# Kernel tuning notes

Measured on AMD Instinct MI355X. Metric: run time of the kernel, lower is better.

Reference implementation:

```python
import jax, jax.numpy as jnp
import numpy as np

H = 16
D_MODEL = 1024
D_K = D_MODEL // H


def setup_inputs() -> dict:
    key = jax.random.key(0)
    ks = jax.random.split(key, 12)
    B, S = 4, 2048
    scale = 1.0 / np.sqrt(D_MODEL)
    inp = {
        "query": jax.random.normal(ks[0], (B, S, D_MODEL), dtype=jnp.float32),
        "key": jax.random.normal(ks[1], (B, S, D_MODEL), dtype=jnp.float32),
        "value": jax.random.normal(ks[2], (B, S, D_MODEL), dtype=jnp.float32),
        "Wq": jax.random.normal(ks[3], (D_MODEL, D_MODEL), dtype=jnp.float32) * scale,
        "bq": jnp.zeros((D_MODEL,), dtype=jnp.float32),
        "Wk": jax.random.normal(ks[4], (D_MODEL, D_MODEL), dtype=jnp.float32) * scale,
        "bk": jnp.zeros((D_MODEL,), dtype=jnp.float32),
        "Wv": jax.random.normal(ks[5], (D_MODEL, D_MODEL), dtype=jnp.float32) * scale,
        "bv": jnp.zeros((D_MODEL,), dtype=jnp.float32),
        "Wo": jax.random.normal(ks[6], (D_MODEL, D_MODEL), dtype=jnp.float32) * scale,
        "bo": jnp.zeros((D_MODEL,), dtype=jnp.float32),
    }
    return inp


def reference(query, key, value, Wq, bq, Wk, bk, Wv, bv, Wo, bo):
    B, S, _ = query.shape
    # Linear projections (torch Linear: x @ W^T + b), then split heads -> [B,H,S,d_k]
    def proj(x, W, b):
        y = x @ W.T + b
        return y.reshape(B, S, H, D_K).transpose(0, 2, 1, 3)

    q = proj(query, Wq, bq)
    k = proj(key, Wk, bk)
    v = proj(value, Wv, bv)

    # Explicit QK^T / sqrt(d_k), softmax, AV (no mask; dropout = identity in eval)
    scores = jnp.einsum("bhqd,bhkd->bhqk", q, k) / jnp.sqrt(jnp.float32(D_K))
    attn = jax.nn.softmax(scores, axis=-1)
    x = jnp.einsum("bhqk,bhkd->bhqd", attn, v)

    # Merge heads and final output projection
    x = x.transpose(0, 2, 1, 3).reshape(B, S, H * D_K)
    return x @ Wo.T + bo
```

## Files before the change

### kernel.cpp

```cpp
#include <hip/hip_runtime.h>
#include <hip/hip_bf16.h>
#include <stdint.h>

#define BATCH 4
#define SEQ   2048
#define DM    1024
#define NH    16
#define DK    64
#define MROWS (BATCH * SEQ)

#define C1 0.1803368801111204f

typedef __attribute__((ext_vector_type(8))) short short8;
typedef __attribute__((ext_vector_type(4))) float f32x4;
typedef __attribute__((ext_vector_type(4))) float floatv4;
typedef __attribute__((ext_vector_type(4))) unsigned short us4;
typedef __attribute__((ext_vector_type(4))) unsigned int uint4v;

static __device__ __forceinline__ unsigned short f2bf(float f) {
    union { float f; uint32_t u; } c; c.f = f;
    uint32_t u = c.u;
    return (unsigned short)((u + 0x7fffu + ((u >> 16) & 1u)) >> 16);
}

static __device__ __forceinline__ unsigned int cvt_pk_bf16(float a, float b) {
    __hip_bfloat162 h = __float22bfloat162_rn(float2{a, b});
    unsigned int u; __builtin_memcpy(&u, &h, 4); return u;
}

static __device__ __forceinline__ float ex2(float x) { return __builtin_amdgcn_exp2f(x); }

#define AS1C(p) ((const __attribute__((address_space(1))) unsigned int*)(uintptr_t)(const void*)(p))
#define AS3(p)  ((__attribute__((address_space(3))) unsigned int*)(uintptr_t)(void*)(p))

__global__ __launch_bounds__(256) void cvt_k(const float* __restrict__ q, const float* __restrict__ k,
                                             const float* __restrict__ v, const float* __restrict__ wq,
                                             const float* __restrict__ wk, const float* __restrict__ wv,
                                             const float* __restrict__ wo,
                                             unsigned short* __restrict__ oq, unsigned short* __restrict__ ok,
                                             unsigned short* __restrict__ ov, unsigned short* __restrict__ owq,
                                             unsigned short* __restrict__ owk, unsigned short* __restrict__ owv,
                                             unsigned short* __restrict__ owo) {
    const int bid = blockIdx.x;
    const float* s;
    unsigned short* o;
    int i;
    if (bid < 24576) {
        const int z = bid >> 13;
        i = (bid & 8191) * 256 + threadIdx.x;
        s = (z == 0) ? q : (z == 1) ? k : v;
        o = (z == 0) ? oq : (z == 1) ? ok : ov;
    } else {
        const int r = bid - 24576;
        const int z = r >> 10;
        i = (r & 1023) * 256 + threadIdx.x;
        s = (z == 0) ? wq : (z == 1) ? wk : (z == 2) ? wv : wo;
        o = (z == 0) ? owq : (z == 1) ? owk : (z == 2) ? owv : owo;
    }
    floatv4 vv = ((const floatv4*)s)[i];
    us4 w; w.x = f2bf(vv.x); w.y = f2bf(vv.y); w.z = f2bf(vv.z); w.w = f2bf(vv.w);
    ((us4*)o)[i] = w;
}

static __device__ __forceinline__ void gemm_body(const unsigned short* __restrict__ A,
                                                 const unsigned short* __restrict__ Bw,
                                                 const float* __restrict__ bias,
                                                 void* __restrict__ out, int m0, int n0,
                                                 float scale, int mode) {
    constexpr int K = DM;
    constexpr int NK = K / 32;

    const int tid = threadIdx.x;
    const int wave = tid >> 6, lane = tid & 63, quad = lane >> 4, l16 = lane & 15;
    const int wm = wave >> 1, wn = wave & 1;

    __shared__ alignas(16) unsigned short As[2][256 * 32];
    __shared__ alignas(16) unsigned short Bs[2][128 * 32];

    f32x4 acc[4][4];
    #pragma unroll
    for (int i = 0; i < 4; i++)
        #pragma unroll
        for (int j = 0; j < 4; j++) acc[i][j] = (f32x4){0.f, 0.f, 0.f, 0.f};

    const int scol8 = (((lane & 3) ^ ((lane >> 3) & 3))) * 8;
    const unsigned short* Ag0 = A  + (size_t)(m0 + wave * 32 + (lane >> 2)) * K + scol8;
    const unsigned short* Ag1 = Ag0 + (size_t)16 * K;
    const unsigned short* Bg0 = Bw + (size_t)(n0 + wave * 16 + (lane >> 2)) * K + scol8;

    const int rsw = (quad ^ ((l16 >> 1) & 3)) * 8;

    short8 af[4], bfr[4];

#define GX_STG(b, kt)                                                                     \
    {   __builtin_amdgcn_global_load_lds(AS1C(Ag0 + (size_t)(kt) * 32),                   \
                                         AS3(&As[b][(wave * 32) * 32]), 16, 0, 0);        \
        __builtin_amdgcn_global_load_lds(AS1C(Ag1 + (size_t)(kt) * 32),                   \
                                         AS3(&As[b][(wave * 32 + 16) * 32]), 16, 0, 0);   \
        __builtin_amdgcn_global_load_lds(AS1C(Bg0 + (size_t)(kt) * 32),                   \
                                         AS3(&Bs[b][(wave * 16) * 32]), 16, 0, 0); }

#define GX_LD(b)                                                                          \
    {   _Pragma("unroll")                                                                 \
        for (int i_ = 0; i_ < 4; i_++) af[i_]  = *(const short8*)&As[b][(wm * 64 + i_ * 16 + l16) * 32 + rsw]; \
        _Pragma("unroll")                                                                 \
        for (int j_ = 0; j_ < 4; j_++) bfr[j_] = *(const short8*)&Bs[b][(wn * 64 + j_ * 16 + l16) * 32 + rsw]; }

#define GX_MMA                                                                            \
    {   __builtin_amdgcn_s_setprio(1);                                                    \
        _Pragma("unroll")                                                                 \
        for (int i_ = 0; i_ < 4; i_++)                                                    \
            _Pragma("unroll")                                                             \
            for (int j_ = 0; j_ < 4; j_++)                                                \
                acc[i_][j_] = __builtin_amdgcn_mfma_f32_16x16x32_bf16(af[i_], bfr[j_], acc[i_][j_], 0, 0, 0); \
        __builtin_amdgcn_s_setprio(0); }

#define GX_VM0  { asm volatile("s_waitcnt vmcnt(0)" ::: "memory"); }
#define GX_BAR  __builtin_amdgcn_s_barrier()
#define GX_SB0  __builtin_amdgcn_sched_barrier(0)
#define GX_LG0  { asm volatile("s_waitcnt lgkmcnt(0)" ::: "memory"); __builtin_amdgcn_sched_barrier(0); }

    GX_STG(0, 0);
    #pragma unroll 1
    for (int k = 0; k < NK; k += 2) {
        GX_VM0; GX_BAR; GX_SB0;
        GX_STG(1, k + 1);
        GX_LD(0); GX_LG0; GX_MMA;
        GX_VM0; GX_BAR; GX_SB0;
        if (k + 2 < NK) GX_STG(0, k + 2);
        GX_LD(1); GX_LG0; GX_MMA;
    }

#undef GX_STG
#undef GX_LD
#undef GX_MMA
#undef GX_VM0
#undef GX_BAR
#undef GX_SB0
#undef GX_LG0

    #pragma unroll
    for (int nf = 0; nf < 4; nf++) {
        const int n = n0 + wn * 64 + nf * 16 + l16;
        const float bv = bias[n];
        if (mode == 2) {
            const int bb = m0 >> 11;
            const int hh = n >> 6, dd = n & (DK - 1);
            unsigned short* obase = (unsigned short*)out
                                  + (((size_t)bb * NH + hh) * DK + dd) * SEQ
                                  + (m0 & (SEQ - 1)) + wm * 64 + quad * 8;
            #pragma unroll
            for (int mf = 0; mf < 4; mf++) {
                us4 w;
                #pragma unroll
                for (int r = 0; r < 4; r++) w[r] = f2bf(acc[mf][nf][r] + bv);
                *(us4*)(obase + (mf >> 1) * 32 + (mf & 1) * 4) = w;
            }
        } else {
            const int hh = n >> 6, dd = n & (DK - 1);
            #pragma unroll
            for (int mf = 0; mf < 4; mf++) {
                #pragma unroll
                for (int r = 0; r < 4; r++) {
                    const int mrow = m0 + wm * 64 + mf * 16 + quad * 4 + r;
                    float val = (acc[mf][nf][r] + bv) * scale;
                    if (mode == 0) {
                        int bb = mrow >> 11, ss = mrow & (SEQ - 1);
                        ((unsigned short*)out)[((((size_t)bb * NH + hh) * SEQ + ss) << 6) + dd] = f2bf(val);
                    } else {
                        ((float*)out)[(size_t)mrow * DM + n] = val;
                    }
                }
            }
        }
    }
}

__global__ __launch_bounds__(512, 4) void gemm_qkv_k(const unsigned short* qa, const unsigned short* ka,
                                                     const unsigned short* va, const unsigned short* wq,
                                                     const unsigned short* wk, const unsigned short* wv,
                                                     const float* bq, const float* bk, const float* bv,
                                                     unsigned short* qh, unsigned short* kh,
                                                     unsigned short* vtc) {
    const int z = blockIdx.z;
    const unsigned short* A = (z == 0) ? qa : (z == 1) ? ka : va;
    const unsigned short* W = (z == 0) ? wq : (z == 1) ? wk : wv;
    const float* bi = (z == 0) ? bq : (z == 1) ? bk : bv;
    void* o = (z == 0) ? (void*)qh : (z == 1) ? (void*)kh : (void*)vtc;
    const float sc = (z == 0) ? C1 : 1.0f;
    const int mode = (z == 2) ? 2 : 0;
    gemm_body(A, W, bi, o, blockIdx.x * 256, blockIdx.y * 128, sc, mode);
}

__global__ __launch_bounds__(512, 4) void gemm_o_k(const unsigned short* xb, const unsigned short* wo,
                                                   const float* bo, float* out) {
    gemm_body(xb, wo, bo, out, blockIdx.x * 256, blockIdx.y * 128, 1.0f, 1);
}

__global__ __launch_bounds__(256, 2) void flash_attn_k(const unsigned short* __restrict__ Qh,
                                                       const unsigned short* __restrict__ Kh,
                                                       const unsigned short* __restrict__ Vtc,
                                                       unsigned short* __restrict__ Xb) {
    const int tid = threadIdx.x;
    const int wave = tid >> 6, lane = tid & 63, quad = lane >> 4, l16 = lane & 15;
    const int h = blockIdx.y, b = blockIdx.z;
    const unsigned short* Qp = Qh  + (size_t)(b * NH + h) * SEQ * DK;
    const unsigned short* Kp = Kh  + (size_t)(b * NH + h) * SEQ * DK;
    const unsigned short* Vp = Vtc + (size_t)(b * NH + h) * DK * SEQ;
    const int q0 = blockIdx.x * 256 + wave * 64;

    __shared__ alignas(16) unsigned short kt[2][128][72];
    __shared__ alignas(16) unsigned short vt[2][64][136];

    short8 aq[4][2];
    #pragma unroll
    for (int m = 0; m < 4; m++)
        #pragma unroll
        for (int kk = 0; kk < 2; kk++)
            aq[m][kk] = *(const short8*)(Qp + (size_t)(q0 + m * 16 + l16) * DK + kk * 32 + quad * 8);

    short8 ones;
    #pragma unroll
    for (int j = 0; j < 8; j++) ones[j] = (short)0x3F80;

    f32x4 O[4][4];
    f32x4 lacc[4];
    #pragma unroll
    for (int m = 0; m < 4; m++) {
        #pragma unroll
        for (int db = 0; db < 4; db++) O[m][db] = (f32x4){0.f, 0.f, 0.f, 0.f};
        lacc[m] = (f32x4){0.f, 0.f, 0.f, 0.f};
    }

    const unsigned short* kgp = Kp + (size_t)(tid >> 3) * DK + (tid & 7) * 8;
    const unsigned short* vgp = Vp + (size_t)(tid >> 4) * SEQ + (tid & 15) * 8;
    unsigned short* kws0 = &kt[0][tid >> 3][(tid & 7) * 8];
    unsigned short* vws0 = &vt[0][tid >> 4][(tid & 15) * 8];

    short8 krg[4], vrg[4];
    #pragma unroll
    for (int it = 0; it < 4; it++) {
        krg[it] = *(const short8*)(kgp + (size_t)it * 32 * DK);
        vrg[it] = *(const short8*)(vgp + (size_t)it * 16 * SEQ);
    }
    kgp += (size_t)128 * DK;
    vgp += 128;
    #pragma unroll
    for (int it = 0; it < 4; it++) {
        *(short8*)(kws0 + it * 32 * 72) = krg[it];
        *(short8*)(vws0 + it * 16 * 136) = vrg[it];
    }
    #pragma unroll
    for (int it = 0; it < 4; it++) {
        krg[it] = *(const short8*)(kgp + (size_t)it * 32 * DK);
        vrg[it] = *(const short8*)(vgp + (size_t)it * 16 * SEQ);
    }
    kgp += (size_t)128 * DK;
    vgp += 128;
    asm volatile("s_waitcnt lgkmcnt(0)" ::: "memory");
    __builtin_amdgcn_s_barrier();
    __builtin_amdgcn_sched_barrier(0);

#define FLASH_TILE(cur)                                                                   \
    {   _Pragma("unroll")                                                                 \
        for (int it = 0; it < 4; it++) {                                                  \
            *(short8*)(kws0 + ((cur) ^ 1) * 128 * 72 + it * 32 * 72) = krg[it];           \
            *(short8*)(vws0 + ((cur) ^ 1) * 64 * 136 + it * 16 * 136) = vrg[it];          \
        }                                                                                 \
        _Pragma("unroll")                                                                 \
        for (int it = 0; it < 4; it++) {                                                  \
            krg[it] = *(const short8*)(kgp + (size_t)it * 32 * DK);                       \
            vrg[it] = *(const short8*)(vgp + (size_t)it * 16 * SEQ);                      \
        }                                                                                 \
        kgp += (size_t)128 * DK;                                                          \
        vgp += 128;                                                                       \
        _Pragma("unroll")                                                                 \
        for (int t = 0; t < 4; t++) {                                                     \
            f32x4 s[4][2];                                                                \
            _Pragma("unroll")                                                             \
            for (int m = 0; m < 4; m++) {                                                 \
                s[m][0] = (f32x4){0.f, 0.f, 0.f, 0.f};                                    \
                s[m][1] = (f32x4){0.f, 0.f, 0.f, 0.f};                                    \
            }                                                                             \
            _Pragma("unroll")                                                             \
            for (int kk = 0; kk < 2; kk++) {                                              \
                short8 bk0 = *(const short8*)&kt[cur][(t * 2    ) * 16 + l16][kk * 32 + quad * 8]; \
                short8 bk1 = *(const short8*)&kt[cur][(t * 2 + 1) * 16 + l16][kk * 32 + quad * 8]; \
                _Pragma("unroll")                                                         \
                for (int m = 0; m < 4; m++) {                                             \
                    s[m][0] = __builtin_amdgcn_mfma_f32_16x16x32_bf16(bk0, aq[m][kk], s[m][0], 0, 0, 0); \
                    s[m][1] = __builtin_amdgcn_mfma_f32_16x16x32_bf16(bk1, aq[m][kk], s[m][1], 0, 0, 0); \
                }                                                                         \
            }                                                                             \
            short8 pa[4];                                                                 \
            _Pragma("unroll")                                                             \
            for (int m = 0; m < 4; m++) {                                                 \
                uint4v pk;                                                                \
                pk.x = cvt_pk_bf16(ex2(s[m][0][0]), ex2(s[m][0][1]));                     \
                pk.y = cvt_pk_bf16(ex2(s[m][0][2]), ex2(s[m][0][3]));                     \
                pk.z = cvt_pk_bf16(ex2(s[m][1][0]), ex2(s[m][1][1]));                     \
                pk.w = cvt_pk_bf16(ex2(s[m][1][2]), ex2(s[m][1][3]));                     \
                __builtin_memcpy(&pa[m], &pk, 16);                                        \
            }                                                                             \
            _Pragma("unroll")                                                             \
            for (int db = 0; db < 4; db++) {                                              \
                short8 vf = *(const short8*)&vt[cur][db * 16 + l16][t * 32 + quad * 8];   \
                _Pragma("unroll")                                                         \
                for (int m = 0; m < 4; m++)                                               \
                    O[m][db] = __builtin_amdgcn_mfma_f32_16x16x32_bf16(pa[m], vf, O[m][db], 0, 0, 0); \
            }                                                                             \
            _Pragma("unroll")                                                             \
            for (int m = 0; m < 4; m++)                                                   \
                lacc[m] = __builtin_amdgcn_mfma_f32_16x16x32_bf16(pa[m], ones, lacc[m], 0, 0, 0); \
        }                                                                                 \
        asm volatile("s_waitcnt lgkmcnt(0)" ::: "memory");                                \
        __builtin_amdgcn_s_barrier();                                                     \
        __builtin_amdgcn_sched_barrier(0);                                                \
    }

    #pragma unroll 1
    for (int ti = 0; ti < SEQ / 128; ti += 2) {
        FLASH_TILE(0);
        FLASH_TILE(1);
    }
#undef FLASH_TILE

    #pragma unroll
    for (int m = 0; m < 4; m++) {
        #pragma unroll
        for (int r = 0; r < 4; r++) {
            const float inv = 1.f / lacc[m][r];
            const int srow = q0 + m * 16 + quad * 4 + r;
            unsigned short* op = Xb + ((size_t)b * SEQ + srow) * DM + h * DK;
            #pragma unroll
            for (int db = 0; db < 4; db++)
                op[db * 16 + l16] = f2bf(O[m][db][r] * inv);
        }
    }
}

extern "C" void kernel_launch(void* const* d_in, const int* in_sizes, int n_in,
                              void* d_out, int out_size, void* d_ws, size_t ws_size,
                              hipStream_t stream) {
    const float* q_in = (const float*)d_in[0];
    const float* k_in = (const float*)d_in[1];
    const float* v_in = (const float*)d_in[2];
    const float* Wq   = (const float*)d_in[3];
    const float* bq   = (const float*)d_in[4];
    const float* Wk   = (const float*)d_in[5];
    const float* bk   = (const float*)d_in[6];
    const float* Wv   = (const float*)d_in[7];
    const float* bv   = (const float*)d_in[8];
    const float* Wo   = (const float*)d_in[9];
    const float* bo   = (const float*)d_in[10];

    const size_t MB = 1024ull * 1024ull;
    char* ws = (char*)d_ws;
    unsigned short* qa  = (unsigned short*)(ws +   0 * MB);
    unsigned short* ka  = (unsigned short*)(ws +  16 * MB);
    unsigned short* va  = (unsigned short*)(ws +  32 * MB);
    unsigned short* wqb = (unsigned short*)(ws +  48 * MB);
    unsigned short* wkb = (unsigned short*)(ws +  50 * MB);
    unsigned short* wvb = (unsigned short*)(ws +  52 * MB);
    unsigned short* wob = (unsigned short*)(ws +  54 * MB);
    unsigned short* qh  = (unsigned short*)(ws +  56 * MB);
    unsigned short* kh  = (unsigned short*)(ws +  72 * MB);
    unsigned short* vtc = (unsigned short*)(ws +  88 * MB);
    unsigned short* xb  = (unsigned short*)(ws + 104 * MB);

    cvt_k<<<dim3(28672), 256, 0, stream>>>(q_in, k_in, v_in, Wq, Wk, Wv, Wo,
                                           qa, ka, va, wqb, wkb, wvb, wob);

    gemm_qkv_k<<<dim3(MROWS / 256, DM / 128, 3), 512, 0, stream>>>(qa, ka, va, wqb, wkb, wvb,
                                                                   bq, bk, bv, qh, kh, vtc);

    flash_attn_k<<<dim3(SEQ / 256, NH, BATCH), 256, 0, stream>>>(qh, kh, vtc, xb);

    gemm_o_k<<<dim3(MROWS / 256, DM / 128), 512, 0, stream>>>(xb, wob, bo, (float*)d_out);
}
```

Measured before the change: 334.2 us.

## Triple-buffer GEMM LDS staging and split conversion kernel into two launches

The shared GEMM body moves from two LDS buffers to three, with a prefetch distance of two K-tiles and a partial vmcnt(3) wait, so one tile's global loads stay in flight while the next is computed. This aims to hide global-to-LDS latency better. It raises LDS use per block (72KB), which may reduce occupancy. The single fp32-to-bf16 conversion kernel is also split into separate 2D-grid launches for activations and weights, adding one launch.

Result: no change. 331.2 us (-0.9%).

```diff
diff --git a/kernel.cpp b/kernel.cpp
--- a/kernel.cpp
+++ b/kernel.cpp
@@ -33,32 +33,29 @@
 #define AS1C(p) ((const __attribute__((address_space(1))) unsigned int*)(uintptr_t)(const void*)(p))
 #define AS3(p)  ((__attribute__((address_space(3))) unsigned int*)(uintptr_t)(void*)(p))
 
-__global__ __launch_bounds__(256) void cvt_k(const float* __restrict__ q, const float* __restrict__ k,
-                                             const float* __restrict__ v, const float* __restrict__ wq,
-                                             const float* __restrict__ wk, const float* __restrict__ wv,
-                                             const float* __restrict__ wo,
-                                             unsigned short* __restrict__ oq, unsigned short* __restrict__ ok,
-                                             unsigned short* __restrict__ ov, unsigned short* __restrict__ owq,
-                                             unsigned short* __restrict__ owk, unsigned short* __restrict__ owv,
-                                             unsigned short* __restrict__ owo) {
-    const int bid = blockIdx.x;
-    const float* s;
-    unsigned short* o;
-    int i;
-    if (bid < 24576) {
-        const int z = bid >> 13;
-        i = (bid & 8191) * 256 + threadIdx.x;
-        s = (z == 0) ? q : (z == 1) ? k : v;
-        o = (z == 0) ? oq : (z == 1) ? ok : ov;
-    } else {
-        const int r = bid - 24576;
-        const int z = r >> 10;
-        i = (r & 1023) * 256 + threadIdx.x;
-        s = (z == 0) ? wq : (z == 1) ? wk : (z == 2) ? wv : wo;
-        o = (z == 0) ? owq : (z == 1) ? owk : (z == 2) ? owv : owo;
-    }
-    floatv4 vv = ((const floatv4*)s)[i];
-    us4 w; w.x = f2bf(vv.x); w.y = f2bf(vv.y); w.z = f2bf(vv.z); w.w = f2bf(vv.w);
+__global__ __launch_bounds__(256) void cvt3_k(const float* __restrict__ a, const float* __restrict__ b,
+                                              const float* __restrict__ c,
+                                              unsigned short* __restrict__ oa, unsigned short* __restrict__ ob,
+                                              unsigned short* __restrict__ oc) {
+    const int z = blockIdx.y;
+    const float* s = (z == 0) ? a : (z == 1) ? b : c;
+    unsigned short* o = (z == 0) ? oa : (z == 1) ? ob : oc;
+    int i = blockIdx.x * 256 + threadIdx.x;
+    floatv4 v = ((const floatv4*)s)[i];
+    us4 w; w.x = f2bf(v.x); w.y = f2bf(v.y); w.z = f2bf(v.z); w.w = f2bf(v.w);
+    ((us4*)o)[i] = w;
+}
+
+__global__ __launch_bounds__(256) void cvt4_k(const float* __restrict__ a, const float* __restrict__ b,
+                                              const float* __restrict__ c, const float* __restrict__ d,
+                                              unsigned short* __restrict__ oa, unsigned short* __restrict__ ob,
+                                              unsigned short* __restrict__ oc, unsigned short* __restrict__ od) {
+    const int z = blockIdx.y;
+    const float* s = (z == 0) ? a : (z == 1) ? b : (z == 2) ? c : d;
+    unsigned short* o = (z == 0) ? oa : (z == 1) ? ob : (z == 2) ? oc : od;
+    int i = blockIdx.x * 256 + threadIdx.x;
+    floatv4 v = ((const floatv4*)s)[i];
+    us4 w; w.x = f2bf(v.x); w.y = f2bf(v.y); w.z = f2bf(v.z); w.w = f2bf(v.w);
     ((us4*)o)[i] = w;
 }
 
@@ -74,8 +71,8 @@
     const int wave = tid >> 6, lane = tid & 63, quad = lane >> 4, l16 = lane & 15;
     const int wm = wave >> 1, wn = wave & 1;
 
-    __shared__ alignas(16) unsigned short As[2][256 * 32];
-    __shared__ alignas(16) unsigned short Bs[2][128 * 32];
+    __shared__ alignas(16) unsigned short As[3][256 * 32];
+    __shared__ alignas(16) unsigned short Bs[3][128 * 32];
 
     f32x4 acc[4][4];
     #pragma unroll
@@ -93,18 +90,22 @@
     short8 af[4], bfr[4];
 
 #define GX_STG(b, kt)                                                                     \
-    {   __builtin_amdgcn_global_load_lds(AS1C(Ag0 + (size_t)(kt) * 32),                   \
-                                         AS3(&As[b][(wave * 32) * 32]), 16, 0, 0);        \
+    {   unsigned short* as_ = &As[b][0];                                                  \
+        unsigned short* bs_ = &Bs[b][0];                                                  \
+        __builtin_amdgcn_global_load_lds(AS1C(Ag0 + (size_t)(kt) * 32),                   \
+                                         AS3(as_ + (wave * 32) * 32), 16, 0, 0);          \
         __builtin_amdgcn_global_load_lds(AS1C(Ag1 + (size_t)(kt) * 32),                   \
-                                         AS3(&As[b][(wave * 32 + 16) * 32]), 16, 0, 0);   \
+                                         AS3(as_ + (wave * 32 + 16) * 32), 16, 0, 0);     \
         __builtin_amdgcn_global_load_lds(AS1C(Bg0 + (size_t)(kt) * 32),                   \
-                                         AS3(&Bs[b][(wave * 16) * 32]), 16, 0, 0); }
+                                         AS3(bs_ + (wave * 16) * 32), 16, 0, 0); }
 
 #define GX_LD(b)                                                                          \
-    {   _Pragma("unroll")                                                                 \
-        for (int i_ = 0; i_ < 4; i_++) af[i_]  = *(const short8*)&As[b][(wm * 64 + i_ * 16 + l16) * 32 + rsw]; \
-        _Pragma("unroll")                                                                 \
-        for (int j_ = 0; j_ < 4; j_++) bfr[j_] = *(const short8*)&Bs[b][(wn * 64 + j_ * 16 + l16) * 32 + rsw]; }
+    {   const unsigned short* ar_ = &As[b][0];                                            \
+        const unsigned short* br_ = &Bs[b][0];                                            \
+        _Pragma("unroll")                                                                 \
+        for (int i_ = 0; i_ < 4; i_++) af[i_]  = *(const short8*)&ar_[(wm * 64 + i_ * 16 + l16) * 32 + rsw]; \
+        _Pragma("unroll")                                                                 \
+        for (int j_ = 0; j_ < 4; j_++) bfr[j_] = *(const short8*)&br_[(wn * 64 + j_ * 16 + l16) * 32 + rsw]; }
 
 #define GX_MMA                                                                            \
     {   __builtin_amdgcn_s_setprio(1);                                                    \
@@ -115,25 +116,32 @@
                 acc[i_][j_] = __builtin_amdgcn_mfma_f32_16x16x32_bf16(af[i_], bfr[j_], acc[i_][j_], 0, 0, 0); \
         __builtin_amdgcn_s_setprio(0); }
 
+#define GX_VM3  { asm volatile("s_waitcnt vmcnt(3)" ::: "memory"); }
 #define GX_VM0  { asm volatile("s_waitcnt vmcnt(0)" ::: "memory"); }
 #define GX_BAR  __builtin_amdgcn_s_barrier()
 #define GX_SB0  __builtin_amdgcn_sched_barrier(0)
 #define GX_LG0  { asm volatile("s_waitcnt lgkmcnt(0)" ::: "memory"); __builtin_amdgcn_sched_barrier(0); }
 
     GX_STG(0, 0);
+    GX_STG(1, 1);
+    int bc = 0;
     #pragma unroll 1
-    for (int k = 0; k < NK; k += 2) {
-        GX_VM0; GX_BAR; GX_SB0;
-        GX_STG(1, k + 1);
-        GX_LD(0); GX_LG0; GX_MMA;
-        GX_VM0; GX_BAR; GX_SB0;
-        if (k + 2 < NK) GX_STG(0, k + 2);
-        GX_LD(1); GX_LG0; GX_MMA;
-    }
+    for (int k = 0; k < NK - 1; ++k) {
+        GX_VM3; GX_BAR; GX_SB0;
+        if (k + 2 < NK) {
+            int bp = bc + 2; if (bp >= 3) bp -= 3;
+            GX_STG(bp, k + 2);
+        }
+        GX_LD(bc); GX_LG0; GX_MMA;
+        bc = (bc == 2) ? 0 : bc + 1;
+    }
+    GX_VM0; GX_BAR; GX_SB0;
+    GX_LD(bc); GX_LG0; GX_MMA;
 
 #undef GX_STG
 #undef GX_LD
 #undef GX_MMA
+#undef GX_VM3
 #undef GX_VM0
 #undef GX_BAR
 #undef GX_SB0
@@ -368,8 +376,8 @@
     unsigned short* vtc = (unsigned short*)(ws +  88 * MB);
     unsigned short* xb  = (unsigned short*)(ws + 104 * MB);
 
-    cvt_k<<<dim3(28672), 256, 0, stream>>>(q_in, k_in, v_in, Wq, Wk, Wv, Wo,
-                                           qa, ka, va, wqb, wkb, wvb, wob);
+    cvt3_k<<<dim3(8192, 3), 256, 0, stream>>>(q_in, k_in, v_in, qa, ka, va);
+    cvt4_k<<<dim3(1024, 4), 256, 0, stream>>>(Wq, Wk, Wv, Wo, wqb, wkb, wvb, wob);
 
     gemm_qkv_k<<<dim3(MROWS / 256, DM / 128, 3), 512, 0, stream>>>(qa, ka, va, wqb, wkb, wvb,
                                                                    bq, bk, bv, qh, kh, vtc);
```
